# Optimization experiments

Hardware: AMD Instinct MI355X
Metric: run time of the kernel (lower is better)

Reference implementation:

```python
import jax, jax.numpy as jnp
import numpy as np
from jax import lax

B, CIN, HW = 4, 3, 256      # batch, image channels, image size
HID = 128                   # hidden_size
EMB_D = 64                  # embedding_dim == encoder output channels
K = 1024                    # num_embeddings
L = 2                       # num encoder/decoder layers (1 resblock each)


def _conv(x, w, b, stride, pad):
    y = lax.conv_general_dilated(x, w, (stride, stride), ((pad, pad), (pad, pad)),
                                 dimension_numbers=('NCHW', 'OIHW', 'NCHW'))
    return y + b[None, :, None, None]


def _bn(x):
    # BatchNorm2d in training mode: batch stats over (N,H,W), affine at init (gamma=1, beta=0)
    m = x.mean((0, 2, 3), keepdims=True)
    v = x.var((0, 2, 3), keepdims=True)
    return (x - m) * lax.rsqrt(v + 1e-5)


def _resblock(x, w1, b1, w2, b2):
    y = jax.nn.relu(_bn(_conv(x, w1, b1, 1, 1)))
    y = _bn(_conv(y, w2, b2, 1, 1))
    return jax.nn.relu(y + x)


def _conv_t(x, w, b):
    # torch ConvTranspose2d(k=4, s=2, p=1); w in torch layout (I, O, 4, 4)
    wf = jnp.flip(w, (2, 3)).transpose(1, 0, 2, 3)  # (O, I, 4, 4)
    y = lax.conv_general_dilated(x, wf, (1, 1), ((2, 2), (2, 2)), lhs_dilation=(2, 2),
                                 dimension_numbers=('NCHW', 'OIHW', 'NCHW'))
    return y + b[None, :, None, None]


def _vqvae(x, enc_in_w, enc_in_b, enc_res_w1, enc_res_b1, enc_res_w2, enc_res_b2,
           enc_down_w, enc_down_b, enc_out_w, enc_out_b,
           dec_in_w, dec_in_b, dec_res_w1, dec_res_b1, dec_res_w2, dec_res_b2,
           dec_up_w, dec_up_b, dec_out_w, dec_out_b, codebook):
    sg = lax.stop_gradient
    # ---- encoder ----
    h = _conv(x, enc_in_w, enc_in_b, 1, 0)
    for i in range(L):
        h = _resblock(h, enc_res_w1[i], enc_res_b1[i], enc_res_w2[i], enc_res_b2[i])
        h = jax.nn.relu(_conv(h, enc_down_w[i], enc_down_b[i], 2, 1))
    z = _conv(h, enc_out_w, enc_out_b, 1, 0)  # (B, C, H/4, W/4)
    # ---- vector quantize ----
    Bz, C, Hl, Wl = z.shape
    zf = z.transpose(0, 2, 3, 1).reshape(-1, C)  # (N, C)
    # ||z - e||^2 expanded; same argmin as the (N,K,C) form without materializing it
    d = (zf * zf).sum(1, keepdims=True) - 2.0 * (zf @ codebook.T) + (codebook * codebook).sum(1)[None, :]
    idx = jnp.argmin(d, axis=1)  # (N,)
    z_q = codebook[idx].reshape(Bz, Hl, Wl, C).transpose(0, 3, 1, 2)
    z_q_st = z_q + sg(z - z_q)  # as in source: forward value == z, grads flow to codebook
    # ---- decoder ----
    h = _conv(z_q_st, dec_in_w, dec_in_b, 1, 0)
    for i in range(L):
        h = _resblock(h, dec_res_w1[i], dec_res_b1[i], dec_res_w2[i], dec_res_b2[i])
        h = jax.nn.relu(_conv_t(h, dec_up_w[i], dec_up_b[i]))
    recon = jax.nn.sigmoid(_conv(h, dec_out_w, dec_out_b, 1, 0))
    # ---- losses ----
    commit = jnp.mean((z - sg(z_q_st)) ** 2)
    cb_l = jnp.mean((sg(z) - z_q_st) ** 2)
    counts = jnp.zeros((K,), jnp.float32).at[idx].add(1.0)
    p = counts + 1e-6
    p = p / p.sum()
    ent = -(p * jnp.log(p)).sum()
    loss = commit + cb_l - ent
    return recon, loss, idx.reshape(Bz, Hl, Wl)


def setup_inputs() -> dict:
    key = jax.random.key(0)
    ks = iter(jax.random.split(key, 40))
    def w(shape, fan_in):
        return jax.random.normal(next(ks), shape, jnp.float32) * np.float32((2.0 / fan_in) ** 0.5)
    z128 = lambda *s: jnp.zeros(s, jnp.float32)
    return {
        'x': jax.random.uniform(next(ks), (B, CIN, HW, HW), jnp.float32),
        'enc_in_w': w((HID, CIN, 1, 1), CIN), 'enc_in_b': z128(HID),
        'enc_res_w1': w((L, HID, HID, 3, 3), HID * 9), 'enc_res_b1': z128(L, HID),
        'enc_res_w2': w((L, HID, HID, 3, 3), HID * 9), 'enc_res_b2': z128(L, HID),
        'enc_down_w': w((L, HID, HID, 4, 4), HID * 16), 'enc_down_b': z128(L, HID),
        'enc_out_w': w((EMB_D, HID, 1, 1), HID), 'enc_out_b': z128(EMB_D),
        'dec_in_w': w((HID, EMB_D, 1, 1), EMB_D), 'dec_in_b': z128(HID),
        'dec_res_w1': w((L, HID, HID, 3, 3), HID * 9), 'dec_res_b1': z128(L, HID),
        'dec_res_w2': w((L, HID, HID, 3, 3), HID * 9), 'dec_res_b2': z128(L, HID),
        'dec_up_w': w((L, HID, HID, 4, 4), HID * 16), 'dec_up_b': z128(L, HID),  # (I,O,4,4) torch layout
        'dec_out_w': w((CIN, HID, 1, 1), HID), 'dec_out_b': z128(CIN),
        'codebook': jax.random.normal(next(ks), (K, EMB_D), jnp.float32) * np.float32((2.0 / (K + EMB_D)) ** 0.5),
    }


def reference(x, enc_in_w, enc_in_b, enc_res_w1, enc_res_b1, enc_res_w2, enc_res_b2,
              enc_down_w, enc_down_b, enc_out_w, enc_out_b,
              dec_in_w, dec_in_b, dec_res_w1, dec_res_b1, dec_res_w2, dec_res_b2,
              dec_up_w, dec_up_b, dec_out_w, dec_out_b, codebook):
    return _vqvae(x, enc_in_w, enc_in_b, enc_res_w1, enc_res_b1, enc_res_w2, enc_res_b2,
                  enc_down_w, enc_down_b, enc_out_w, enc_out_b,
                  dec_in_w, dec_in_b, dec_res_w1, dec_res_b1, dec_res_w2, dec_res_b2,
                  dec_up_w, dec_up_b, dec_out_w, dec_out_b, codebook)
```

## Files before the change

kernel.cpp:

```cpp
#include <hip/hip_runtime.h>
#include <math.h>


#define RE_SIZE 786432

typedef float f32x4 __attribute__((ext_vector_type(4)));
typedef short bf16x8 __attribute__((ext_vector_type(8)));

__device__ __forceinline__ unsigned short f2bf(float f) {
  unsigned u = __float_as_uint(f);
  return (unsigned short)((u + 0x7fffu + ((u >> 16) & 1u)) >> 16);
}
__device__ __forceinline__ float bf2f(unsigned short h) {
  return __uint_as_float(((unsigned)h) << 16);
}
__device__ __forceinline__ void split3(float v, unsigned short& a,
                                       unsigned short& b, unsigned short& c) {
  a = f2bf(v); float r = v - bf2f(a);
  b = f2bf(r); r -= bf2f(b);
  c = f2bf(r);
}

__global__ __launch_bounds__(256) void wsplit_kernel(
    const float* __restrict__ w, unsigned short* __restrict__ w0,
    unsigned short* __restrict__ w1, unsigned short* __restrict__ w2) {
  int id = blockIdx.x * 256 + threadIdx.x;
  int j = id & 7, lane = (id >> 3) & 63, rest = id >> 9;
  int mt = rest & 7, rest2 = rest >> 3;
  int tap = rest2 % 9, cc = rest2 / 9;
  int co = mt * 16 + (lane & 15);
  int ci = cc * 32 + (lane >> 4) * 8 + j;
  float v = w[((long)co * 128 + ci) * 9 + tap];
  unsigned short a, b, c; split3(v, a, b, c);
  w0[id] = a; w1[id] = b; w2[id] = c;
}

__global__ __launch_bounds__(256) void wsplit4_kernel(
    const float* __restrict__ w, unsigned short* __restrict__ w0,
    unsigned short* __restrict__ w1, unsigned short* __restrict__ w2) {
  int id = blockIdx.x * 256 + threadIdx.x;
  int j = id & 7, lane = (id >> 3) & 63;
  int mt = (id >> 9) & 7, pair = (id >> 12) & 7, cc = id >> 15;
  int q = lane >> 4;
  int tap = pair * 2 + (q >> 1);
  int ky = tap >> 2, kx = tap & 3;
  int co = mt * 16 + (lane & 15);
  int ci = cc * 16 + (q & 1) * 8 + j;
  float v = w[((long)co * 128 + ci) * 16 + ky * 4 + kx];
  unsigned short a, b, c; split3(v, a, b, c);
  w0[id] = a; w1[id] = b; w2[id] = c;
}

__global__ __launch_bounds__(256) void wsplitT_kernel(
    const float* __restrict__ w, unsigned short* __restrict__ w0,
    unsigned short* __restrict__ w1) {
  int id = blockIdx.x * 256 + threadIdx.x;
  int jj = id & 7, lane = (id >> 3) & 63;
  int mt = (id >> 9) & 7, j = (id >> 12) & 3, cls = (id >> 14) & 3, cc = id >> 16;
  int py = cls >> 1, px = cls & 1, jy = j >> 1, jx = j & 1;
  int ky = py ? (jy ? 2 : 0) : (jy ? 3 : 1);
  int kx = px ? (jx ? 2 : 0) : (jx ? 3 : 1);
  int co = mt * 16 + (lane & 15);
  int ci = cc * 32 + (lane >> 4) * 8 + jj;
  float v = w[((long)ci * 128 + co) * 16 + ky * 4 + kx];
  unsigned short h = f2bf(v);
  w0[id] = h;
  w1[id] = f2bf(v - bf2f(h));
}

template<int IMODE, int SPLIT>
__global__ __launch_bounds__(256) void conv3x3_mfma_kernel(
    const float* __restrict__ in, const unsigned short* __restrict__ w0s,
    const unsigned short* __restrict__ w1s, const unsigned short* __restrict__ w2s,
    const float* __restrict__ bias, float* __restrict__ out, int H, int W,
    const float2* __restrict__ mr, const float* __restrict__ xin,
    const float* __restrict__ w1, const float* __restrict__ b1) {
  __shared__ __align__(16) unsigned short s_x[SPLIT][5760];
  int tid = threadIdx.x, wv = tid >> 6, lane = tid & 63;
  int q = lane >> 4, c15 = lane & 15;
  int tilesX = W >> 4;
  int tx0 = (blockIdx.x % tilesX) << 4;
  int ty0 = (blockIdx.x / tilesX) << 3;
  int n = blockIdx.z;
  long HWl = (long)H * W;
  long ibase = (long)n * 128 * HWl;
  f32x4 acc[2][8];
#pragma unroll
  for (int a = 0; a < 2; ++a)
#pragma unroll
    for (int b = 0; b < 8; ++b) acc[a][b] = (f32x4){0.f, 0.f, 0.f, 0.f};

  for (int cc = 0; cc < 4; ++cc) {
    __syncthreads();
    for (int l = tid; l < 720; l += 256) {
      int cig = l / 180, px = l % 180;
      int y = px / 18, x = px % 18;
      int gy = ty0 + y - 1, gx = tx0 + x - 1;
      float v[8];
      if ((unsigned)gy < (unsigned)H && (unsigned)gx < (unsigned)W) {
        if (IMODE == 2) {
          const float* xp = xin + (long)n * 3 * HWl + (long)gy * W + gx;
          float x0 = xp[0], x1 = xp[HWl], x2 = xp[2 * HWl];
#pragma unroll
          for (int c = 0; c < 8; ++c) {
            int ci = cc * 32 + cig * 8 + c;
            v[c] = fmaf(w1[ci * 3 + 0], x0,
                   fmaf(w1[ci * 3 + 1], x1,
                   fmaf(w1[ci * 3 + 2], x2, b1[ci])));
          }
        } else {
          const float* ip = in + ibase + (long)(cc * 32 + cig * 8) * HWl
                            + (long)gy * W + gx;
#pragma unroll
          for (int c = 0; c < 8; ++c) v[c] = ip[(long)c * HWl];
          if (IMODE == 1) {
#pragma unroll
            for (int c = 0; c < 8; ++c) {
              float2 s = mr[cc * 32 + cig * 8 + c];
              v[c] = fmaxf((v[c] - s.x) * s.y, 0.f);
            }
          }
        }
      } else {
#pragma unroll
        for (int c = 0; c < 8; ++c) v[c] = 0.f;
      }
      bf16x8 sv[SPLIT];
#pragma unroll
      for (int c = 0; c < 8; ++c) {
        unsigned short h0 = f2bf(v[c]); float r = v[c] - bf2f(h0);
        unsigned short h1 = f2bf(r);
        sv[0][c] = (short)h0; sv[1][c] = (short)h1;
        if (SPLIT == 3) { r -= bf2f(h1); sv[2][c] = (short)f2bf(r); }
      }
#pragma unroll
      for (int s = 0; s < SPLIT; ++s) *(bf16x8*)(s_x[s] + l * 8) = sv[s];
    }
    __syncthreads();

    for (int tap = 0; tap < 9; ++tap) {
      int dy = tap / 3, dx = tap % 3;
      long fbase = (long)((cc * 9 + tap) * 8) * 64;
      bf16x8 a0[2], a1[2], a2[2];
#pragma unroll
      for (int m = 0; m < 2; ++m) {
        long fi = fbase + (2 * wv + m) * 64 + lane;
        a0[m] = ((const bf16x8*)w0s)[fi];
        a1[m] = ((const bf16x8*)w1s)[fi];
        if (SPLIT == 3) a2[m] = ((const bf16x8*)w2s)[fi];
      }
      int xoff = (q * 180 + dy * 18 + c15 + dx) * 8;
#pragma unroll
      for (int nn = 0; nn < 8; ++nn) {
        bf16x8 b0 = *(const bf16x8*)(s_x[0] + xoff + nn * 144);
        bf16x8 b1v = *(const bf16x8*)(s_x[1] + xoff + nn * 144);
#pragma unroll
        for (int m = 0; m < 2; ++m) {
          acc[m][nn] = __builtin_amdgcn_mfma_f32_16x16x32_bf16(a0[m], b0, acc[m][nn], 0, 0, 0);
          acc[m][nn] = __builtin_amdgcn_mfma_f32_16x16x32_bf16(a0[m], b1v, acc[m][nn], 0, 0, 0);
          acc[m][nn] = __builtin_amdgcn_mfma_f32_16x16x32_bf16(a1[m], b0, acc[m][nn], 0, 0, 0);
        }
        if (SPLIT == 3) {
          bf16x8 b2 = *(const bf16x8*)(s_x[2] + xoff + nn * 144);
#pragma unroll
          for (int m = 0; m < 2; ++m) {
            acc[m][nn] = __builtin_amdgcn_mfma_f32_16x16x32_bf16(a0[m], b2, acc[m][nn], 0, 0, 0);
            acc[m][nn] = __builtin_amdgcn_mfma_f32_16x16x32_bf16(a1[m], b1v, acc[m][nn], 0, 0, 0);
            acc[m][nn] = __builtin_amdgcn_mfma_f32_16x16x32_bf16(a2[m], b0, acc[m][nn], 0, 0, 0);
          }
        }
      }
    }
  }
#pragma unroll
  for (int mt2 = 0; mt2 < 2; ++mt2) {
    int co0 = (wv * 2 + mt2) * 16 + q * 4;
#pragma unroll
    for (int nn = 0; nn < 8; ++nn) {
      long pxoff = ibase + (long)(ty0 + nn) * W + tx0 + c15;
#pragma unroll
      for (int r = 0; r < 4; ++r)
        out[pxoff + (long)(co0 + r) * HWl] = acc[mt2][nn][r] + bias[co0 + r];
    }
  }
}

__global__ __launch_bounds__(256) void down_mfma_kernel(
    const float* __restrict__ in, const unsigned short* __restrict__ w0s,
    const unsigned short* __restrict__ w1s, const unsigned short* __restrict__ w2s,
    const float* __restrict__ bias, float* __restrict__ out, int Hin, int Win) {
  __shared__ __align__(16) unsigned short s_x[3][9792];
  int tid = threadIdx.x, wv = tid >> 6, lane = tid & 63;
  int q = lane >> 4, c15 = lane & 15;
  int Hout = Hin >> 1, Wout = Win >> 1;
  int tilesX = Wout >> 4;
  int tx0 = (blockIdx.x % tilesX) << 4;
  int ty0 = (blockIdx.x / tilesX) << 3;
  int n = blockIdx.z;
  long HWin = (long)Hin * Win, HWout = (long)Hout * Wout;
  long ibase = (long)n * 128 * HWin, obase = (long)n * 128 * HWout;
  f32x4 acc[2][8];
#pragma unroll
  for (int a = 0; a < 2; ++a)
#pragma unroll
    for (int b = 0; b < 8; ++b) acc[a][b] = (f32x4){0.f, 0.f, 0.f, 0.f};

  for (int cc = 0; cc < 8; ++cc) {
    __syncthreads();
    for (int l = tid; l < 1224; l += 256) {
      int cig = l / 612, rem = l % 612;
      int g = rem / 153, p = rem % 153;
      int py = p / 17, px_ = p % 17;
      int gy = g >> 1, gx = g & 1;
      int iy = 2 * (ty0 + py - gy) + gy;
      int ix = 2 * (tx0 + px_ - gx) + gx;
      float v[8];
      if ((unsigned)iy < (unsigned)Hin && (unsigned)ix < (unsigned)Win) {
        const float* ip = in + ibase + (long)(cc * 16 + cig * 8) * HWin
                          + (long)iy * Win + ix;
#pragma unroll
        for (int c = 0; c < 8; ++c) v[c] = ip[(long)c * HWin];
      } else {
#pragma unroll
        for (int c = 0; c < 8; ++c) v[c] = 0.f;
      }
      bf16x8 s0, s1, s2;
#pragma unroll
      for (int c = 0; c < 8; ++c) {
        unsigned short h0, h1, h2; split3(v[c], h0, h1, h2);
        s0[c] = (short)h0; s1[c] = (short)h1; s2[c] = (short)h2;
      }
      *(bf16x8*)(s_x[0] + l * 8) = s0;
      *(bf16x8*)(s_x[1] + l * 8) = s1;
      *(bf16x8*)(s_x[2] + l * 8) = s2;
    }
    __syncthreads();

    for (int pr = 0; pr < 8; ++pr) {
      long fbase = (long)((cc * 8 + pr) * 8) * 64;
      bf16x8 a0[2], a1[2], a2[2];
#pragma unroll
      for (int m = 0; m < 2; ++m) {
        long fi = fbase + (2 * wv + m) * 64 + lane;
        a0[m] = ((const bf16x8*)w0s)[fi];
        a1[m] = ((const bf16x8*)w1s)[fi];
        a2[m] = ((const bf16x8*)w2s)[fi];
      }
      int tap = pr * 2 + (q >> 1);
      int ky = tap >> 2, kx = tap & 3;
      int gy = (ky + 1) & 1, gx = (kx + 1) & 1;
      int dy = (ky == 0) ? -1 : ((ky == 3) ? 1 : 0);
      int dx = (kx == 0) ? -1 : ((kx == 3) ? 1 : 0);
      int g = gy * 2 + gx, cig = q & 1;
      int xoff = ((cig * 4 + g) * 153 + (dy + gy) * 17 + (c15 + dx + gx)) * 8;
#pragma unroll
      for (int nn = 0; nn < 8; ++nn) {
        bf16x8 b0 = *(const bf16x8*)(s_x[0] + xoff + nn * 136);
        bf16x8 b1v = *(const bf16x8*)(s_x[1] + xoff + nn * 136);
        bf16x8 b2 = *(const bf16x8*)(s_x[2] + xoff + nn * 136);
#pragma unroll
        for (int m = 0; m < 2; ++m) {
          acc[m][nn] = __builtin_amdgcn_mfma_f32_16x16x32_bf16(a0[m], b0, acc[m][nn], 0, 0, 0);
          acc[m][nn] = __builtin_amdgcn_mfma_f32_16x16x32_bf16(a0[m], b1v, acc[m][nn], 0, 0, 0);
          acc[m][nn] = __builtin_amdgcn_mfma_f32_16x16x32_bf16(a1[m], b0, acc[m][nn], 0, 0, 0);
          acc[m][nn] = __builtin_amdgcn_mfma_f32_16x16x32_bf16(a0[m], b2, acc[m][nn], 0, 0, 0);
          acc[m][nn] = __builtin_amdgcn_mfma_f32_16x16x32_bf16(a1[m], b1v, acc[m][nn], 0, 0, 0);
          acc[m][nn] = __builtin_amdgcn_mfma_f32_16x16x32_bf16(a2[m], b0, acc[m][nn], 0, 0, 0);
        }
      }
    }
  }
#pragma unroll
  for (int mt2 = 0; mt2 < 2; ++mt2) {
    int co0 = (wv * 2 + mt2) * 16 + q * 4;
#pragma unroll
    for (int nn = 0; nn < 8; ++nn) {
      long pxoff = obase + (long)(ty0 + nn) * Wout + tx0 + c15;
#pragma unroll
      for (int r = 0; r < 4; ++r)
        out[pxoff + (long)(co0 + r) * HWout] =
            fmaxf(acc[mt2][nn][r] + bias[co0 + r], 0.f);
    }
  }
}

__global__ __launch_bounds__(256) void up_mfma_kernel(
    const float* __restrict__ in, const unsigned short* __restrict__ wh,
    const unsigned short* __restrict__ wl, const float* __restrict__ bias,
    float* __restrict__ out, int Hin, int Win) {
  __shared__ __align__(16) unsigned short s_xh[5760];
  __shared__ __align__(16) unsigned short s_xl[5760];
  int tid = threadIdx.x, wv = tid >> 6, lane = tid & 63;
  int q = lane >> 4, c15 = lane & 15;
  int cls = blockIdx.z & 3, n = blockIdx.z >> 2;
  int py = cls >> 1, px = cls & 1;
  int Hout = Hin << 1, Wout = Win << 1;
  int tilesX = Win >> 4;
  int x0 = (blockIdx.x % tilesX) << 4;
  int m0 = (blockIdx.x / tilesX) << 3;
  long HWin = (long)Hin * Win, HWout = (long)Hout * Wout;
  long ibase = (long)n * 128 * HWin, obase = (long)n * 128 * HWout;
  f32x4 acc[2][8];
#pragma unroll
  for (int a = 0; a < 2; ++a)
#pragma unroll
    for (int b = 0; b < 8; ++b) acc[a][b] = (f32x4){0.f, 0.f, 0.f, 0.f};

  for (int cc = 0; cc < 4; ++cc) {
    __syncthreads();
    for (int l = tid; l < 720; l += 256) {
      int cig = l / 180, p = l % 180;
      int y = p / 18, x = p % 18;
      int gy = m0 + y - 1, gx = x0 + x - 1;
      float v[8];
      if ((unsigned)gy < (unsigned)Hin && (unsigned)gx < (unsigned)Win) {
        const float* ip = in + ibase + (long)(cc * 32 + cig * 8) * HWin
                          + (long)gy * Win + gx;
#pragma unroll
        for (int c = 0; c < 8; ++c) v[c] = ip[(long)c * HWin];
      } else {
#pragma unroll
        for (int c = 0; c < 8; ++c) v[c] = 0.f;
      }
      bf16x8 hv, lv;
#pragma unroll
      for (int c = 0; c < 8; ++c) {
        unsigned short h = f2bf(v[c]);
        hv[c] = (short)h;
        lv[c] = (short)f2bf(v[c] - bf2f(h));
      }
      *(bf16x8*)(s_xh + l * 8) = hv;
      *(bf16x8*)(s_xl + l * 8) = lv;
    }
    __syncthreads();

#pragma unroll
    for (int j = 0; j < 4; ++j) {
      int jy = j >> 1, jx = j & 1;
      int dy = py ? (jy ? 0 : 1) : (jy ? -1 : 0);
      int dx = px ? (jx ? 0 : 1) : (jx ? -1 : 0);
      long fbase = (long)((((cc * 4 + cls) * 4 + j) * 8)) * 64;
      const bf16x8* aph = (const bf16x8*)wh + fbase;
      const bf16x8* apl = (const bf16x8*)wl + fbase;
      bf16x8 ah0 = aph[(2 * wv) * 64 + lane];
      bf16x8 ah1 = aph[(2 * wv + 1) * 64 + lane];
      bf16x8 al0 = apl[(2 * wv) * 64 + lane];
      bf16x8 al1 = apl[(2 * wv + 1) * 64 + lane];
      int xoff = (q * 180 + (dy + 1) * 18 + (c15 + dx + 1)) * 8;
#pragma unroll
      for (int nn = 0; nn < 8; ++nn) {
        bf16x8 bh = *(const bf16x8*)(s_xh + xoff + nn * 144);
        bf16x8 bl = *(const bf16x8*)(s_xl + xoff + nn * 144);
        acc[0][nn] = __builtin_amdgcn_mfma_f32_16x16x32_bf16(ah0, bh, acc[0][nn], 0, 0, 0);
        acc[0][nn] = __builtin_amdgcn_mfma_f32_16x16x32_bf16(ah0, bl, acc[0][nn], 0, 0, 0);
        acc[0][nn] = __builtin_amdgcn_mfma_f32_16x16x32_bf16(al0, bh, acc[0][nn], 0, 0, 0);
        acc[1][nn] = __builtin_amdgcn_mfma_f32_16x16x32_bf16(ah1, bh, acc[1][nn], 0, 0, 0);
        acc[1][nn] = __builtin_amdgcn_mfma_f32_16x16x32_bf16(ah1, bl, acc[1][nn], 0, 0, 0);
        acc[1][nn] = __builtin_amdgcn_mfma_f32_16x16x32_bf16(al1, bh, acc[1][nn], 0, 0, 0);
      }
    }
  }
#pragma unroll
  for (int mt2 = 0; mt2 < 2; ++mt2) {
    int co0 = (wv * 2 + mt2) * 16 + q * 4;
#pragma unroll
    for (int nn = 0; nn < 8; ++nn) {
      long pxoff = obase + (long)(2 * (m0 + nn) + py) * Wout + 2 * (x0 + c15) + px;
#pragma unroll
      for (int r = 0; r < 4; ++r)
        out[pxoff + (long)(co0 + r) * HWout] =
            fmaxf(acc[mt2][nn][r] + bias[co0 + r], 0.f);
    }
  }
}

template<int ACT, int CW>
__global__ __launch_bounds__(256) void conv1x1_kernel(
    const float* __restrict__ in, const float* __restrict__ w,
    const float* __restrict__ bias, float* __restrict__ out,
    int N, int Cin, int Cout, int HW) {
  extern __shared__ float wl[];
  int co0 = blockIdx.y * CW;
  for (int i = threadIdx.x; i < CW * Cin; i += blockDim.x)
    wl[i] = w[(long)co0 * Cin + i];
  __syncthreads();
  int HW4 = HW >> 2;
  long p4 = (long)blockIdx.x * blockDim.x + threadIdx.x;
  if (p4 >= (long)N * HW4) return;
  int n = (int)(p4 / HW4), hw4 = (int)(p4 % HW4);
  const float4* inp = (const float4*)(in + (long)n * Cin * HW) + hw4;
  float4* outp = (float4*)(out + (long)n * Cout * HW) + hw4;
  float4 acc[CW];
#pragma unroll
  for (int j = 0; j < CW; ++j) { float bb = bias[co0 + j]; acc[j] = make_float4(bb, bb, bb, bb); }
  for (int ci = 0; ci < Cin; ++ci) {
    float4 v = inp[(long)ci * HW4];
#pragma unroll
    for (int j = 0; j < CW; ++j) {
      float ww = wl[j * Cin + ci];
      acc[j].x = fmaf(ww, v.x, acc[j].x);
      acc[j].y = fmaf(ww, v.y, acc[j].y);
      acc[j].z = fmaf(ww, v.z, acc[j].z);
      acc[j].w = fmaf(ww, v.w, acc[j].w);
    }
  }
#pragma unroll
  for (int j = 0; j < CW; ++j) {
    float4 v = acc[j];
    if (ACT == 2) {
      v.x = 1.f / (1.f + expf(-v.x));
      v.y = 1.f / (1.f + expf(-v.y));
      v.z = 1.f / (1.f + expf(-v.z));
      v.w = 1.f / (1.f + expf(-v.w));
    }
    outp[(long)(co0 + j) * HW4] = v;
  }
}

__global__ __launch_bounds__(256) void bn_part_kernel(
    const float* __restrict__ x, float2* __restrict__ part, int HW) {
  int c = blockIdx.x, sl = blockIdx.y, tid = threadIdx.x;
  int seg = HW >> 3;
  double s = 0.0, ss = 0.0;
  for (int n = 0; n < 4; ++n) {
    const float4* xp = (const float4*)(x + ((long)(n * 128 + c)) * HW + (long)sl * seg);
    for (int i = tid; i < (seg >> 2); i += 256) {
      float4 v = xp[i];
      s  += (double)v.x + (double)v.y + (double)v.z + (double)v.w;
      ss += (double)v.x * v.x + (double)v.y * v.y + (double)v.z * v.z + (double)v.w * v.w;
    }
  }
  __shared__ double shs[256], shss[256];
  shs[tid] = s; shss[tid] = ss;
  __syncthreads();
  for (int off = 128; off > 0; off >>= 1) {
    if (tid < off) { shs[tid] += shs[tid + off]; shss[tid] += shss[tid + off]; }
    __syncthreads();
  }
  if (tid == 0) part[c * 8 + sl] = make_float2((float)shs[0], (float)shss[0]);
}

__global__ __launch_bounds__(128) void bn_final_kernel(
    const float2* __restrict__ part, float2* __restrict__ mr, float cntf) {
  int c = threadIdx.x;
  if (c < 128) {
    double s = 0.0, ss = 0.0;
#pragma unroll
    for (int i = 0; i < 8; ++i) { float2 p = part[c * 8 + i]; s += p.x; ss += p.y; }
    double cnt = (double)cntf;
    double m = s / cnt;
    double var = ss / cnt - m * m;
    mr[c] = make_float2((float)m, (float)(1.0 / sqrt(var + 1e-5)));
  }
}

template<int RMODE>
__global__ __launch_bounds__(256) void bn_res_relu_kernel(
    float* __restrict__ y, const float2* __restrict__ mr,
    const float* __restrict__ res,
    const float* __restrict__ xin, const float* __restrict__ w1,
    const float* __restrict__ b1, int HW4) {
  int nc = blockIdx.y;
  int c = nc & 127, n = nc >> 7;
  float2 s = mr[c];
  int i = blockIdx.x * blockDim.x + threadIdx.x;
  if (i >= HW4) return;
  long off = (long)nc * HW4 + i;
  float4 v = ((const float4*)y)[off];
  v.x = (v.x - s.x) * s.y; v.y = (v.y - s.x) * s.y;
  v.z = (v.z - s.x) * s.y; v.w = (v.w - s.x) * s.y;
  float4 r4;
  if (RMODE == 0) {
    r4 = ((const float4*)res)[off];
  } else {
    const float4* xp = (const float4*)(xin) + (long)n * 3 * HW4 + i;
    float4 x0 = xp[0], x1 = xp[HW4], x2 = xp[2 * HW4];
    float wa = w1[c * 3 + 0], wb = w1[c * 3 + 1], wc = w1[c * 3 + 2], bb = b1[c];
    r4.x = fmaf(wa, x0.x, fmaf(wb, x1.x, fmaf(wc, x2.x, bb)));
    r4.y = fmaf(wa, x0.y, fmaf(wb, x1.y, fmaf(wc, x2.y, bb)));
    r4.z = fmaf(wa, x0.z, fmaf(wb, x1.z, fmaf(wc, x2.z, bb)));
    r4.w = fmaf(wa, x0.w, fmaf(wb, x1.w, fmaf(wc, x2.w, bb)));
  }
  v.x = fmaxf(v.x + r4.x, 0.f); v.y = fmaxf(v.y + r4.y, 0.f);
  v.z = fmaxf(v.z + r4.z, 0.f); v.w = fmaxf(v.w + r4.w, 0.f);
  ((float4*)y)[off] = v;
}

__global__ __launch_bounds__(256) void vq_kernel(
    const float* __restrict__ z, const float* __restrict__ cb,
    float* __restrict__ idx_out, float* __restrict__ counts, int HWl) {
  __shared__ float s_z[64][65];
  __shared__ float s_cb[64][64];
  __shared__ float s_bd[4][64];
  __shared__ int   s_bk[4][64];
  int tid = threadIdx.x;
  int r0 = blockIdx.x * 64;
  for (int l = tid; l < 64 * 64; l += 256) {
    int c = l >> 6, rs = l & 63;
    int r = r0 + rs;
    int n = r / HWl, rem = r % HWl;
    s_z[rs][c] = z[((long)(n * 64 + c)) * HWl + rem];
  }
  int row = tid & 63, cg = tid >> 6;
  float best = 3.4e38f; int bestk = 0;
  for (int k0 = 0; k0 < 1024; k0 += 64) {
    __syncthreads();
    for (int l = tid; l < 4096; l += 256)
      s_cb[l >> 6][l & 63] = cb[(long)(k0 + (l >> 6)) * 64 + (l & 63)];
    __syncthreads();
#pragma unroll
    for (int j = 0; j < 16; ++j) {
      int kk = cg * 16 + j;
      const float* zp = s_z[row];
      const float* cp = s_cb[kk];
      float d = 0.f;
#pragma unroll
      for (int c = 0; c < 64; ++c) {
        float t = zp[c] - cp[c];
        d = fmaf(t, t, d);
      }
      int k = k0 + kk;
      if (d < best) { best = d; bestk = k; }
    }
  }
  s_bd[cg][row] = best; s_bk[cg][row] = bestk;
  __syncthreads();
  if (tid < 64) {
    float bd = s_bd[0][tid]; int bk = s_bk[0][tid];
#pragma unroll
    for (int g = 1; g < 4; ++g) {
      float d2 = s_bd[g][tid]; int k2 = s_bk[g][tid];
      if (d2 < bd || (d2 == bd && k2 < bk)) { bd = d2; bk = k2; }
    }
    idx_out[r0 + tid] = (float)bk;
    atomicAdd(&counts[bk], 1.0f);
  }
}

__global__ __launch_bounds__(256) void zero_kernel(float* __restrict__ p, int n) {
  int i = blockIdx.x * 256 + threadIdx.x;
  if (i < n) p[i] = 0.f;
}

__global__ __launch_bounds__(256) void entropy_kernel(
    const float* __restrict__ counts, float* __restrict__ loss_out) {
  __shared__ double sh[256];
  int tid = threadIdx.x;
  double s = 0.0;
  for (int i = tid; i < 1024; i += 256) s += (double)counts[i] + 1e-6;
  sh[tid] = s; __syncthreads();
  for (int off = 128; off > 0; off >>= 1) {
    if (tid < off) sh[tid] += sh[tid + off];
    __syncthreads();
  }
  double S = sh[0];
  __syncthreads();
  double pl = 0.0;
  for (int i = tid; i < 1024; i += 256) {
    double p = ((double)counts[i] + 1e-6) / S;
    pl += p * log(p);
  }
  sh[tid] = pl; __syncthreads();
  for (int off = 128; off > 0; off >>= 1) {
    if (tid < off) sh[tid] += sh[tid + off];
    __syncthreads();
  }
  if (tid == 0) loss_out[0] = (float)sh[0];
}

extern "C" void kernel_launch(void* const* d_in, const int* in_sizes, int n_in,
                              void* d_out, int out_size, void* d_ws, size_t ws_size,
                              hipStream_t stream) {
  (void)in_sizes; (void)n_in; (void)out_size; (void)ws_size;
  const float* x          = (const float*)d_in[0];
  const float* enc_in_w   = (const float*)d_in[1];
  const float* enc_in_b   = (const float*)d_in[2];
  const float* enc_res_w1 = (const float*)d_in[3];
  const float* enc_res_b1 = (const float*)d_in[4];
  const float* enc_res_w2 = (const float*)d_in[5];
  const float* enc_res_b2 = (const float*)d_in[6];
  const float* enc_down_w = (const float*)d_in[7];
  const float* enc_down_b = (const float*)d_in[8];
  const float* enc_out_w  = (const float*)d_in[9];
  const float* enc_out_b  = (const float*)d_in[10];
  const float* dec_in_w   = (const float*)d_in[11];
  const float* dec_in_b   = (const float*)d_in[12];
  const float* dec_res_w1 = (const float*)d_in[13];
  const float* dec_res_b1 = (const float*)d_in[14];
  const float* dec_res_w2 = (const float*)d_in[15];
  const float* dec_res_b2 = (const float*)d_in[16];
  const float* dec_up_w   = (const float*)d_in[17];
  const float* dec_up_b   = (const float*)d_in[18];
  const float* dec_out_w  = (const float*)d_in[19];
  const float* dec_out_b  = (const float*)d_in[20];
  const float* codebook   = (const float*)d_in[21];
  float* out = (float*)d_out;

  const long BIG = 33554432;
  const long S1 = 8388608, S2 = 16777216, S3 = 25165824;
  float* P0 = (float*)d_ws;
  float* P1 = P0 + BIG;
  float2* mr   = (float2*)out;
  float* hist  = out + 256;
  float2* part = (float2*)(out + 1280);
  unsigned short* W0 = (unsigned short*)(out + 4096);
  unsigned short* W1 = (unsigned short*)(out + 135168);
  unsigned short* W2 = (unsigned short*)(out + 266240);

  const int W3 = 128 * 128 * 9, W4 = 128 * 128 * 16, BS = 128;
  const dim3 g256(512, 1, 4), g128(128, 1, 4), g64(32, 1, 4);

  wsplit_kernel<<<576, 256, 0, stream>>>(enc_res_w1, W0, W1, W2);
  conv3x3_mfma_kernel<2, 3><<<g256, 256, 0, stream>>>(
      nullptr, W0, W1, W2, enc_res_b1, P0, 256, 256, nullptr, x, enc_in_w, enc_in_b);
  bn_part_kernel<<<dim3(128, 8), 256, 0, stream>>>(P0, part, 65536);
  bn_final_kernel<<<1, 128, 0, stream>>>(part, mr, 262144.f);
  wsplit_kernel<<<576, 256, 0, stream>>>(enc_res_w2, W0, W1, W2);
  conv3x3_mfma_kernel<1, 3><<<g256, 256, 0, stream>>>(
      P0, W0, W1, W2, enc_res_b2, P1, 256, 256, mr, nullptr, nullptr, nullptr);
  bn_part_kernel<<<dim3(128, 8), 256, 0, stream>>>(P1, part, 65536);
  bn_final_kernel<<<1, 128, 0, stream>>>(part, mr, 262144.f);
  bn_res_relu_kernel<1><<<dim3(64, 512), 256, 0, stream>>>(
      P1, mr, nullptr, x, enc_in_w, enc_in_b, 16384);
  wsplit4_kernel<<<1024, 256, 0, stream>>>(enc_down_w, W0, W1, W2);
  down_mfma_kernel<<<g128, 256, 0, stream>>>(P1, W0, W1, W2, enc_down_b, P0, 256, 256);

  wsplit_kernel<<<576, 256, 0, stream>>>(enc_res_w1 + W3, W0, W1, W2);
  conv3x3_mfma_kernel<0, 3><<<g128, 256, 0, stream>>>(
      P0, W0, W1, W2, enc_res_b1 + BS, P0 + S1, 128, 128, nullptr, nullptr, nullptr, nullptr);
  bn_part_kernel<<<dim3(128, 8), 256, 0, stream>>>(P0 + S1, part, 16384);
  bn_final_kernel<<<1, 128, 0, stream>>>(part, mr, 65536.f);
  wsplit_kernel<<<576, 256, 0, stream>>>(enc_res_w2 + W3, W0, W1, W2);
  conv3x3_mfma_kernel<1, 3><<<g128, 256, 0, stream>>>(
      P0 + S1, W0, W1, W2, enc_res_b2 + BS, P0 + S2, 128, 128, mr, nullptr, nullptr, nullptr);
  bn_part_kernel<<<dim3(128, 8), 256, 0, stream>>>(P0 + S2, part, 16384);
  bn_final_kernel<<<1, 128, 0, stream>>>(part, mr, 65536.f);
  bn_res_relu_kernel<0><<<dim3(16, 512), 256, 0, stream>>>(
      P0 + S2, mr, P0, nullptr, nullptr, nullptr, 4096);
  wsplit4_kernel<<<1024, 256, 0, stream>>>(enc_down_w + W4, W0, W1, W2);
  down_mfma_kernel<<<g64, 256, 0, stream>>>(P0 + S2, W0, W1, W2, enc_down_b + BS, P0 + S3, 128, 128);

  conv1x1_kernel<0, 16><<<dim3(16, 4), 256, 16 * 128 * 4, stream>>>(
      P0 + S3, enc_out_w, enc_out_b, P1, 4, 128, 64, 4096);

  zero_kernel<<<4, 256, 0, stream>>>(hist, 1024);
  vq_kernel<<<256, 256, 0, stream>>>(P1, codebook, out + RE_SIZE + 1, hist, 4096);
  entropy_kernel<<<1, 256, 0, stream>>>(hist, out + RE_SIZE);

  conv1x1_kernel<0, 16><<<dim3(16, 8), 256, 16 * 64 * 4, stream>>>(
      P1, dec_in_w, dec_in_b, P0, 4, 64, 128, 4096);

  wsplit_kernel<<<576, 256, 0, stream>>>(dec_res_w1, W0, W1, W2);
  conv3x3_mfma_kernel<0, 2><<<g64, 256, 0, stream>>>(
      P0, W0, W1, W2, dec_res_b1, P0 + S1, 64, 64, nullptr, nullptr, nullptr, nullptr);
  bn_part_kernel<<<dim3(128, 8), 256, 0, stream>>>(P0 + S1, part, 4096);
  bn_final_kernel<<<1, 128, 0, stream>>>(part, mr, 16384.f);
  wsplit_kernel<<<576, 256, 0, stream>>>(dec_res_w2, W0, W1, W2);
  conv3x3_mfma_kernel<1, 2><<<g64, 256, 0, stream>>>(
      P0 + S1, W0, W1, W2, dec_res_b2, P0 + S2, 64, 64, mr, nullptr, nullptr, nullptr);
  bn_part_kernel<<<dim3(128, 8), 256, 0, stream>>>(P0 + S2, part, 4096);
  bn_final_kernel<<<1, 128, 0, stream>>>(part, mr, 16384.f);
  bn_res_relu_kernel<0><<<dim3(4, 512), 256, 0, stream>>>(
      P0 + S2, mr, P0, nullptr, nullptr, nullptr, 1024);
  wsplitT_kernel<<<1024, 256, 0, stream>>>(dec_up_w, W0, W1);
  up_mfma_kernel<<<dim3(32, 1, 16), 256, 0, stream>>>(
      P0 + S2, W0, W1, dec_up_b, P0 + S3, 64, 64);

  wsplit_kernel<<<576, 256, 0, stream>>>(dec_res_w1 + W3, W0, W1, W2);
  conv3x3_mfma_kernel<0, 2><<<g128, 256, 0, stream>>>(
      P0 + S3, W0, W1, W2, dec_res_b1 + BS, P1, 128, 128, nullptr, nullptr, nullptr, nullptr);
  bn_part_kernel<<<dim3(128, 8), 256, 0, stream>>>(P1, part, 16384);
  bn_final_kernel<<<1, 128, 0, stream>>>(part, mr, 65536.f);
  wsplit_kernel<<<576, 256, 0, stream>>>(dec_res_w2 + W3, W0, W1, W2);
  conv3x3_mfma_kernel<1, 2><<<g128, 256, 0, stream>>>(
      P1, W0, W1, W2, dec_res_b2 + BS, P1 + S1, 128, 128, mr, nullptr, nullptr, nullptr);
  bn_part_kernel<<<dim3(128, 8), 256, 0, stream>>>(P1 + S1, part, 16384);
  bn_final_kernel<<<1, 128, 0, stream>>>(part, mr, 65536.f);
  bn_res_relu_kernel<0><<<dim3(16, 512), 256, 0, stream>>>(
      P1 + S1, mr, P0 + S3, nullptr, nullptr, nullptr, 4096);
  wsplitT_kernel<<<1024, 256, 0, stream>>>(dec_up_w + W4, W0, W1);
  up_mfma_kernel<<<dim3(128, 1, 16), 256, 0, stream>>>(
      P1 + S1, W0, W1, dec_up_b + BS, P0, 128, 128);

  conv1x1_kernel<2, 3><<<dim3(256, 1), 256, 3 * 128 * 4, stream>>>(
      P0, dec_out_w, dec_out_b, out, 4, 128, 3, 65536);
}
```

Baseline: 1.906 ms.

## Fold 1x1 input conv into first 3x3 resblock conv weights

Precomposes the encoder's 1x1 input conv (3 channels plus bias) with the first 3x3 resblock conv into effective weights over 36 inputs (9 taps by 4 channels, including a constant-one channel for the bias). The first conv then reads the 3-channel image directly instead of building 128-channel inputs, which cuts its K dimension from 1152 to 36. Border handling stays correct because padded pixels hold a zero in the bias channel too. Precision is kept with a three-way bf16 split and double-precision weight composition.

```diff
diff --git a/kernel.cpp b/kernel.cpp
--- a/kernel.cpp
+++ b/kernel.cpp
@@ -6,6 +6,7 @@
 
 typedef float f32x4 __attribute__((ext_vector_type(4)));
 typedef short bf16x8 __attribute__((ext_vector_type(8)));
+typedef short bf16x4 __attribute__((ext_vector_type(4)));
 
 __device__ __forceinline__ unsigned short f2bf(float f) {
   unsigned u = __float_as_uint(f);
@@ -19,6 +20,123 @@
   a = f2bf(v); float r = v - bf2f(a);
   b = f2bf(r); r -= bf2f(b);
   c = f2bf(r);
+}
+
+__global__ __launch_bounds__(256) void weff_kernel(
+    const float* __restrict__ w3, const float* __restrict__ ew,
+    const float* __restrict__ eb, unsigned short* __restrict__ f0,
+    unsigned short* __restrict__ f1, unsigned short* __restrict__ f2) {
+  int id = blockIdx.x * 256 + threadIdx.x;
+  int j = id & 7, lane = (id >> 3) & 63, mt = (id >> 9) & 7, kc = id >> 12;
+  int co = mt * 16 + (lane & 15);
+  int q = lane >> 4;
+  int k = kc * 32 + q * 8 + j;
+  int t = k >> 2, c = k & 3;
+  float v = 0.f;
+  if (t <= 8) {
+    double acc = 0.0;
+    for (int ci = 0; ci < 128; ++ci) {
+      double wv = (double)w3[((long)co * 128 + ci) * 9 + t];
+      double xv = (c < 3) ? (double)ew[ci * 3 + c] : (double)eb[ci];
+      acc += wv * xv;
+    }
+    v = (float)acc;
+  }
+  unsigned short a, b, cc; split3(v, a, b, cc);
+  f0[id] = a; f1[id] = b; f2[id] = cc;
+}
+
+__global__ __launch_bounds__(256) void conv36_mfma_kernel(
+    const float* __restrict__ xin, const unsigned short* __restrict__ f0,
+    const unsigned short* __restrict__ f1, const unsigned short* __restrict__ f2,
+    const float* __restrict__ bias, float* __restrict__ out, int H, int W) {
+  __shared__ __align__(16) unsigned short s_x[3][720];
+  int tid = threadIdx.x, wv = tid >> 6, lane = tid & 63;
+  int q = lane >> 4, c15 = lane & 15;
+  int tilesX = W >> 4;
+  int tx0 = (blockIdx.x % tilesX) << 4;
+  int ty0 = (blockIdx.x / tilesX) << 3;
+  int n = blockIdx.z;
+  long HWl = (long)H * W;
+  long ibase = (long)n * 128 * HWl;
+  long xbase = (long)n * 3 * HWl;
+  f32x4 acc[2][8];
+#pragma unroll
+  for (int a = 0; a < 2; ++a)
+#pragma unroll
+    for (int b = 0; b < 8; ++b) acc[a][b] = (f32x4){0.f, 0.f, 0.f, 0.f};
+
+  for (int l = tid; l < 180; l += 256) {
+    int y = l / 18, x = l % 18;
+    int gy = ty0 + y - 1, gx = tx0 + x - 1;
+    float v[4] = {0.f, 0.f, 0.f, 0.f};
+    if ((unsigned)gy < (unsigned)H && (unsigned)gx < (unsigned)W) {
+      const float* xp = xin + xbase + (long)gy * W + gx;
+      v[0] = xp[0]; v[1] = xp[HWl]; v[2] = xp[2 * HWl]; v[3] = 1.f;
+    }
+    bf16x4 s0, s1, s2;
+#pragma unroll
+    for (int c = 0; c < 4; ++c) {
+      unsigned short h0, h1, h2; split3(v[c], h0, h1, h2);
+      s0[c] = (short)h0; s1[c] = (short)h1; s2[c] = (short)h2;
+    }
+    *(bf16x4*)(s_x[0] + l * 4) = s0;
+    *(bf16x4*)(s_x[1] + l * 4) = s1;
+    *(bf16x4*)(s_x[2] + l * 4) = s2;
+  }
+  __syncthreads();
+
+#pragma unroll
+  for (int kc = 0; kc < 2; ++kc) {
+    bf16x8 a0[2], a1[2], a2[2];
+#pragma unroll
+    for (int m = 0; m < 2; ++m) {
+      long fi = (long)(kc * 8 + 2 * wv + m) * 64 + lane;
+      a0[m] = ((const bf16x8*)f0)[fi];
+      a1[m] = ((const bf16x8*)f1)[fi];
+      a2[m] = ((const bf16x8*)f2)[fi];
+    }
+    int ta = kc * 8 + 2 * q; if (ta > 8) ta = 8;
+    int tb = ta + 1;         if (tb > 8) tb = 8;
+    int pa_d = (ta / 3) * 18 + ta % 3;
+    int pb_d = (tb / 3) * 18 + tb % 3;
+#pragma unroll
+    for (int nn = 0; nn < 8; ++nn) {
+      int pa = (nn * 18 + c15 + pa_d) * 4;
+      int pb = (nn * 18 + c15 + pb_d) * 4;
+      bf16x8 b0, b1v, b2;
+      bf16x4 lo, hi;
+      lo = *(const bf16x4*)(s_x[0] + pa); hi = *(const bf16x4*)(s_x[0] + pb);
+#pragma unroll
+      for (int i = 0; i < 4; ++i) { b0[i] = lo[i]; b0[4 + i] = hi[i]; }
+      lo = *(const bf16x4*)(s_x[1] + pa); hi = *(const bf16x4*)(s_x[1] + pb);
+#pragma unroll
+      for (int i = 0; i < 4; ++i) { b1v[i] = lo[i]; b1v[4 + i] = hi[i]; }
+      lo = *(const bf16x4*)(s_x[2] + pa); hi = *(const bf16x4*)(s_x[2] + pb);
+#pragma unroll
+      for (int i = 0; i < 4; ++i) { b2[i] = lo[i]; b2[4 + i] = hi[i]; }
+#pragma unroll
+      for (int m = 0; m < 2; ++m) {
+        acc[m][nn] = __builtin_amdgcn_mfma_f32_16x16x32_bf16(a0[m], b0, acc[m][nn], 0, 0, 0);
+        acc[m][nn] = __builtin_amdgcn_mfma_f32_16x16x32_bf16(a0[m], b1v, acc[m][nn], 0, 0, 0);
+        acc[m][nn] = __builtin_amdgcn_mfma_f32_16x16x32_bf16(a1[m], b0, acc[m][nn], 0, 0, 0);
+        acc[m][nn] = __builtin_amdgcn_mfma_f32_16x16x32_bf16(a0[m], b2, acc[m][nn], 0, 0, 0);
+        acc[m][nn] = __builtin_amdgcn_mfma_f32_16x16x32_bf16(a1[m], b1v, acc[m][nn], 0, 0, 0);
+        acc[m][nn] = __builtin_amdgcn_mfma_f32_16x16x32_bf16(a2[m], b0, acc[m][nn], 0, 0, 0);
+      }
+    }
+  }
+#pragma unroll
+  for (int mt2 = 0; mt2 < 2; ++mt2) {
+    int co0 = (wv * 2 + mt2) * 16 + q * 4;
+#pragma unroll
+    for (int nn = 0; nn < 8; ++nn) {
+      long pxoff = ibase + (long)(ty0 + nn) * W + tx0 + c15;
+#pragma unroll
+      for (int r = 0; r < 4; ++r)
+        out[pxoff + (long)(co0 + r) * HWl] = acc[mt2][nn][r] + bias[co0 + r];
+    }
+  }
 }
 
 __global__ __launch_bounds__(256) void wsplit_kernel(
@@ -606,13 +724,16 @@
   unsigned short* W0 = (unsigned short*)(out + 4096);
   unsigned short* W1 = (unsigned short*)(out + 135168);
   unsigned short* W2 = (unsigned short*)(out + 266240);
+  unsigned short* F0 = (unsigned short*)(out + 401408);
+  unsigned short* F1 = F0 + 8192;
+  unsigned short* F2 = F1 + 8192;
 
   const int W3 = 128 * 128 * 9, W4 = 128 * 128 * 16, BS = 128;
   const dim3 g256(512, 1, 4), g128(128, 1, 4), g64(32, 1, 4);
 
-  wsplit_kernel<<<576, 256, 0, stream>>>(enc_res_w1, W0, W1, W2);
-  conv3x3_mfma_kernel<2, 3><<<g256, 256, 0, stream>>>(
-      nullptr, W0, W1, W2, enc_res_b1, P0, 256, 256, nullptr, x, enc_in_w, enc_in_b);
+  weff_kernel<<<32, 256, 0, stream>>>(enc_res_w1, enc_in_w, enc_in_b, F0, F1, F2);
+  conv36_mfma_kernel<<<g256, 256, 0, stream>>>(
+      x, F0, F1, F2, enc_res_b1, P0, 256, 256);
   bn_part_kernel<<<dim3(128, 8), 256, 0, stream>>>(P0, part, 65536);
   bn_final_kernel<<<1, 128, 0, stream>>>(part, mr, 262144.f);
   wsplit_kernel<<<576, 256, 0, stream>>>(enc_res_w2, W0, W1, W2);
```

After: 1.651 ms. 1.15x faster.
